# Kernel optimization log

Hardware: AMD Instinct MI355X
Metric: run time of the kernel (lower is better)

## Reference

```python
import jax, jax.numpy as jnp
import numpy as np

B, S, H = 2, 4096, 1024
NH, BS, NR = 16, 64, 3
HD = H // NH
NB = S // BS
PEN = -10000.0


def setup_inputs():
    key = jax.random.key(0)
    k0, k1, k2, k3 = jax.random.split(key, 4)
    s = 0.02
    inp = {
        'hidden_states': jax.random.normal(k0, (B, S, H), jnp.float32),
        'attention_mask': jnp.ones((B, S), jnp.float32),
        'Wq': jax.random.normal(k1, (H, H), jnp.float32) * s,
        'Wk': jax.random.normal(k2, (H, H), jnp.float32) * s,
        'Wv': jax.random.normal(k3, (H, H), jnp.float32) * s,
        'bq': jnp.zeros((H,), jnp.float32),
        'bk': jnp.zeros((H,), jnp.float32),
        'bv': jnp.zeros((H,), jnp.float32),
    }
    rng = np.random.default_rng(0)
    inp['rand_attn'] = jnp.asarray(rng.integers(1, NB - 1, size=(B, NH, NB - 2, NR)), jnp.int32)
    return inp


def _attend(q_blk, kmat, vmat, mask, rsd):
    # q_blk:[b,h,q,d]  kmat/vmat:[b,h,k,d]  mask: multiplicative {0,1} broadcastable to [b,h,q,k]
    p = jnp.einsum('bhqd,bhkd->bhqk', q_blk, kmat) * rsd + (1.0 - mask) * PEN
    return jnp.einsum('bhqk,bhkd->bhqd', jax.nn.softmax(p, axis=-1), vmat)


def reference(hidden_states, attention_mask, Wq, bq, Wk, bk, Wv, bv, rand_attn):
    b, s, _ = hidden_states.shape
    h, d, bs = NH, HD, BS
    nb = s // bs
    rsd = 1.0 / jnp.sqrt(jnp.asarray(d, hidden_states.dtype))

    def proj(W, bias):
        return (hidden_states @ W + bias).reshape(b, s, h, d).transpose(0, 2, 1, 3)

    q, k, v = proj(Wq, bq), proj(Wk, bk), proj(Wv, bv)  # [b,h,s,d]

    # --- masks (create_masks_for_block_sparse_attn)
    bm = attention_mask.reshape(b, nb, bs)
    band_mask = jnp.einsum('blq,blk->blqk', bm[:, 2:-2],
                           jnp.concatenate([bm[:, 1:-3], bm[:, 2:-2], bm[:, 3:-1]], axis=2))[:, None]
    from_mask = attention_mask.reshape(b, 1, s, 1)
    to_mask = attention_mask.reshape(b, 1, 1, s)

    qb = q.reshape(b, h, nb, bs, d)
    kb = k.reshape(b, h, nb, bs, d)
    vb = v.reshape(b, h, nb, bs, d)

    # --- gather random blocks (jax_gather with batch_dims=2)
    gather2 = jax.vmap(jax.vmap(lambda m, i: m[i]))
    gk = gather2(kb, rand_attn).reshape(b, h, nb - 2, NR * bs, d)
    gv = gather2(vb, rand_attn).reshape(b, h, nb - 2, NR * bs, d)
    rm = jax.vmap(lambda m, i: m[i])(bm, rand_attn).reshape(b, h, nb - 2, NR * bs)
    rand_mask = jnp.einsum('blq,bhlk->bhlqk', bm[:, 1:-1], rm)  # [b,h,nb-2,bs,NR*bs]

    # --- block 0: attends to everything
    first_ctx = _attend(qb[:, :, 0], k, v, to_mask, rsd)[:, :, None]

    # --- block 1: first 3 blocks + last block + its random blocks
    ones_r = jnp.ones((b, 1, 1, NR * bs), q.dtype)
    sk = jnp.concatenate([kb[:, :, 0], kb[:, :, 1], kb[:, :, 2], kb[:, :, -1], gk[:, :, 0]], axis=2)
    sv = jnp.concatenate([vb[:, :, 0], vb[:, :, 1], vb[:, :, 2], vb[:, :, -1], gv[:, :, 0]], axis=2)
    seq_pad = jnp.concatenate([to_mask[:, :, :, :3 * bs], to_mask[:, :, :, -bs:], ones_r], axis=3)
    rand_pad = jnp.concatenate([jnp.ones((b, h, bs, 4 * bs), q.dtype), rand_mask[:, :, 0]], axis=3)
    second_ctx = _attend(qb[:, :, 1], sk, sv, jnp.minimum(seq_pad, rand_pad), rsd)[:, :, None]

    # --- middle blocks 2..nb-3: sliding band + random + first-global + last-global
    mq = qb[:, :, 2:-2]  # [b,h,L,bs,d], L = nb-4
    ek = jnp.concatenate([kb[:, :, 1:-3], kb[:, :, 2:-2], kb[:, :, 3:-1]], axis=3)  # [b,h,L,3bs,d]
    ev = jnp.concatenate([vb[:, :, 1:-3], vb[:, :, 2:-2], vb[:, :, 3:-1]], axis=3)
    band_p = jnp.einsum('bhlqd,bhlkd->bhlqk', mq, ek) * rsd + (1.0 - band_mask) * PEN
    rand_p = jnp.einsum('bhlqd,bhlkd->bhlqk', mq, gk[:, :, 1:-1]) * rsd + (1.0 - rand_mask[:, :, 1:-1]) * PEN
    first_p = jnp.einsum('bhlqd,bhkd->bhlqk', mq, kb[:, :, 0]) * rsd \
        + (1.0 - to_mask[:, :, :, :bs][:, :, :, None]) * PEN
    last_p = jnp.einsum('bhlqd,bhkd->bhlqk', mq, kb[:, :, -1]) * rsd \
        + (1.0 - to_mask[:, :, :, -bs:][:, :, :, None]) * PEN
    # scores layout: [first(bs) | band(3bs) | rand(NR*bs) | last(bs)]
    w = jax.nn.softmax(jnp.concatenate([first_p, band_p, rand_p, last_p], axis=-1), axis=-1)
    mid_ctx = jnp.einsum('bhlqk,bhlkd->bhlqd', w[..., bs:4 * bs], ev)
    mid_ctx += jnp.einsum('bhlqk,bhlkd->bhlqd', w[..., 4 * bs:-bs], gv[:, :, 1:-1])
    mid_ctx += jnp.einsum('bhlqk,bhkd->bhlqd', w[..., :bs], vb[:, :, 0])
    mid_ctx += jnp.einsum('bhlqk,bhkd->bhlqd', w[..., -bs:], vb[:, :, -1])

    # --- block nb-2: first block + last 3 blocks + its random blocks
    slk = jnp.concatenate([kb[:, :, 0], kb[:, :, -3], kb[:, :, -2], kb[:, :, -1], gk[:, :, -1]], axis=2)
    slv = jnp.concatenate([vb[:, :, 0], vb[:, :, -3], vb[:, :, -2], vb[:, :, -1], gv[:, :, -1]], axis=2)
    seq_pad = jnp.concatenate([to_mask[:, :, :, :bs], to_mask[:, :, :, -3 * bs:], ones_r], axis=3)
    rand_pad = jnp.concatenate([jnp.ones((b, h, bs, 4 * bs), q.dtype), rand_mask[:, :, -1]], axis=3)
    seclast_ctx = _attend(qb[:, :, -2], slk, slv, jnp.minimum(seq_pad, rand_pad), rsd)[:, :, None]

    # --- last block: attends to everything
    last_ctx = _attend(qb[:, :, -1], k, v, to_mask, rsd)[:, :, None]

    ctx = jnp.concatenate([first_ctx, second_ctx, mid_ctx, seclast_ctx, last_ctx], axis=2)
    ctx = ctx.reshape(b, h, s, d) * from_mask
    return ctx.transpose(0, 2, 1, 3).reshape(b, s, h * d)
```

## Files before the change

kernel.cpp:

```cpp
#include <hip/hip_runtime.h>

typedef unsigned short u16;
typedef short short8 __attribute__((ext_vector_type(8)));
typedef float f32x4 __attribute__((ext_vector_type(4)));

#define S_TOT 4096
#define NHEAD 16
#define HD 64
#define NB 64
#define BS 64
#define M0 16.0f

__device__ __forceinline__ u16 f2bf(float f) {
    unsigned int u = __builtin_bit_cast(unsigned int, f);
    unsigned int r = (u + 0x7fffu + ((u >> 16) & 1u)) >> 16;
    return (u16)r;
}

__device__ __forceinline__ void gload_lds16(const void* g, void* l) {
    __builtin_amdgcn_global_load_lds(
        (const __attribute__((address_space(1))) unsigned int*)g,
        (__attribute__((address_space(3))) unsigned int*)l, 16, 0, 0);
}

__device__ __forceinline__ float rsum16(float v) {
    v += __shfl_xor(v, 1);
    v += __shfl_xor(v, 2);
    v += __shfl_xor(v, 4);
    v += __shfl_xor(v, 8);
    return v;
}

__global__ __launch_bounds__(256) void convH(const float* __restrict__ h, u16* __restrict__ A) {
    size_t i = (size_t)blockIdx.x * blockDim.x + threadIdx.x;
    float4 v = ((const float4*)h)[i];
    ushort4 o;
    o.x = f2bf(v.x); o.y = f2bf(v.y); o.z = f2bf(v.z); o.w = f2bf(v.w);
    ((ushort4*)A)[i] = o;
}

__global__ __launch_bounds__(256) void transW(const float* __restrict__ Wq,
                                              const float* __restrict__ Wk,
                                              const float* __restrict__ Wv,
                                              u16* __restrict__ Wt) {
    const float* W = blockIdx.z == 0 ? Wq : (blockIdx.z == 1 ? Wk : Wv);
    u16* T = Wt + (size_t)blockIdx.z * 1024 * 1024;
    __shared__ float tile[64][65];
    int n0 = blockIdx.x * 64, k0 = blockIdx.y * 64;
    int tx = threadIdx.x, ty = threadIdx.y;
    for (int r = ty; r < 64; r += 4) tile[r][tx] = W[(size_t)(k0 + r) * 1024 + n0 + tx];
    __syncthreads();
    for (int r = ty; r < 64; r += 4) T[(size_t)(n0 + r) * 1024 + k0 + tx] = f2bf(tile[tx][r]);
}

__global__ __launch_bounds__(256, 2) void gemm_fused(const u16* __restrict__ Ah, const u16* __restrict__ Wt,
                                                     const float* __restrict__ bq, const float* __restrict__ bk,
                                                     const float* __restrict__ bv,
                                                     u16* __restrict__ Qb, u16* __restrict__ Kb,
                                                     u16* __restrict__ Vtb) {
    __shared__ alignas(16) char lds[2][32768];

    int bid = blockIdx.x;
    int xcd = bid & 7, idx = bid >> 3;
    int bm = xcd * 8 + (idx & 7);
    int bn = idx >> 3;
    int m0 = bm * 128, n0 = bn * 128;
    int mode = bn >> 3;
    const float* bias = mode == 0 ? bq : (mode == 1 ? bk : bv);
    int tid = threadIdx.x, wave = tid >> 6, lane = tid & 63;
    int lo = lane & 15, hi = lane >> 4;
    int wr = wave >> 1, wc = wave & 1;

    const char* Ac = (const char*)Ah;
    const char* Wc = (const char*)Wt;

    auto STAGE = [&](int buf, int t) {
#pragma unroll
        for (int i = 0; i < 4; i++) {
            int off = i * 4096 + tid * 16;
            int row = off >> 7, cb = off & 127;
            int cs = cb ^ ((row & 7) << 4);
            char* d = lds[buf] + i * 4096 + wave * 1024;
            gload_lds16(Ac + (size_t)(m0 + row) * 2048 + t * 128 + cs, d);
            gload_lds16(Wc + (size_t)(n0 + row) * 2048 + t * 128 + cs, d + 16384);
        }
    };

    f32x4 acc[4][4];
#pragma unroll
    for (int i = 0; i < 4; i++)
#pragma unroll
        for (int j = 0; j < 4; j++) acc[i][j] = f32x4{0.f, 0.f, 0.f, 0.f};

    STAGE(0, 0);
    asm volatile("s_waitcnt vmcnt(0)" ::: "memory");
    __builtin_amdgcn_s_barrier();
    __builtin_amdgcn_sched_barrier(0);

    for (int t = 0; t < 16; t++) {
        int buf = t & 1;
        if (t < 15) STAGE(buf ^ 1, t + 1);
        const char* As = lds[buf];
        const char* Bs = lds[buf] + 16384;
        short8 b[4][2];
#pragma unroll
        for (int ni = 0; ni < 4; ni++) {
            int row = wc * 64 + ni * 16 + lo;
            int sw = (row & 7) << 4;
#pragma unroll
            for (int kk = 0; kk < 2; kk++)
                b[ni][kk] = *(const short8*)(Bs + row * 128 + ((kk * 64 + hi * 16) ^ sw));
        }
        __builtin_amdgcn_s_setprio(1);
#pragma unroll
        for (int mi = 0; mi < 4; mi++) {
            int row = wr * 64 + mi * 16 + lo;
            int sw = (row & 7) << 4;
            short8 a0 = *(const short8*)(As + row * 128 + ((hi * 16) ^ sw));
            short8 a1 = *(const short8*)(As + row * 128 + ((64 + hi * 16) ^ sw));
#pragma unroll
            for (int ni = 0; ni < 4; ni++) {
                acc[mi][ni] = __builtin_amdgcn_mfma_f32_16x16x32_bf16(a0, b[ni][0], acc[mi][ni], 0, 0, 0);
                acc[mi][ni] = __builtin_amdgcn_mfma_f32_16x16x32_bf16(a1, b[ni][1], acc[mi][ni], 0, 0, 0);
            }
        }
        __builtin_amdgcn_s_setprio(0);
        asm volatile("s_waitcnt vmcnt(0)" ::: "memory");
        __builtin_amdgcn_s_barrier();
        __builtin_amdgcn_sched_barrier(0);
    }

    char* Cs = lds[0];
    int nb0 = n0 & 1023;
    float bv4[4];
#pragma unroll
    for (int ni = 0; ni < 4; ni++) bv4[ni] = bias[nb0 + wc * 64 + ni * 16 + lo];

    if (mode < 2) {
#pragma unroll
        for (int mi = 0; mi < 4; mi++)
#pragma unroll
            for (int ni = 0; ni < 4; ni++)
#pragma unroll
                for (int r = 0; r < 4; r++) {
                    int row = wr * 64 + mi * 16 + hi * 4 + r;
                    int nl = wc * 64 + ni * 16 + lo;
                    *(u16*)(Cs + ((row * 256 + nl * 2) ^ ((row & 7) << 4))) = f2bf(acc[mi][ni][r] + bv4[ni]);
                }
        __syncthreads();
        u16* T = (mode == 0) ? Qb : Kb;
#pragma unroll
        for (int it = 0; it < 8; it++) {
            int off = it * 4096 + tid * 16;
            int row = off >> 8, c = off & 255;
            short8 v = *(const short8*)(Cs + ((row * 256 + c) ^ ((row & 7) << 4)));
            int nm = nb0 + (c >> 1);
            int hh = nm >> 6, d = nm & 63;
            int s = m0 + row;
            int b_ = s >> 12, sr = s & 4095;
            *(short8*)&T[(((size_t)b_ * NHEAD + hh) * S_TOT + sr) * HD + d] = v;
        }
    } else {
#pragma unroll
        for (int mi = 0; mi < 4; mi++)
#pragma unroll
            for (int ni = 0; ni < 4; ni++)
#pragma unroll
                for (int r = 0; r < 4; r++) {
                    int row = wc * 64 + ni * 16 + lo;
                    int ml = wr * 64 + mi * 16 + hi * 4 + r;
                    *(u16*)(Cs + ((row * 256 + ml * 2) ^ ((row & 7) << 4))) = f2bf(acc[mi][ni][r] + bv4[ni]);
                }
        __syncthreads();
#pragma unroll
        for (int it = 0; it < 8; it++) {
            int off = it * 4096 + tid * 16;
            int row = off >> 8, c = off & 255;
            short8 v = *(const short8*)(Cs + ((row * 256 + c) ^ ((row & 7) << 4)));
            int dr = nb0 + row;
            int hh = dr >> 6, d = dr & 63;
            int s = m0 + (c >> 1);
            int b_ = s >> 12, sr = s & 4095;
            *(short8*)&Vtb[(((size_t)b_ * NHEAD + hh) * HD + d) * S_TOT + sr] = v;
        }
    }
}

__global__ __launch_bounds__(256) void bigbird_attn(const u16* __restrict__ Qb, const u16* __restrict__ Kb,
                                                    const u16* __restrict__ Vtb, const float* __restrict__ am,
                                                    const int* __restrict__ rand_attn, float* __restrict__ out,
                                                    float* __restrict__ po, float* __restrict__ pl) {
    int pid = blockIdx.x;
    int xcd = pid & 7, slot = pid >> 3;
    int bh = xcd * 4 + slot / 78;
    int lx = slot % 78;
    int b = bh >> 4, h = bh & 15;
    bool heavy = lx < 16;
    int p = lx & 7;
    int l = heavy ? ((lx >> 3) ? 63 : 0) : (lx - 15);
    const u16* Qh = Qb + (size_t)bh * S_TOT * HD;
    const u16* Kh = Kb + (size_t)bh * S_TOT * HD;
    const u16* Vh = Vtb + (size_t)bh * HD * S_TOT;
    int tid = threadIdx.x, wave = tid >> 6, lane = tid & 63;
    int lo = lane & 15, hi = lane >> 4;

    __shared__ int klist[64];
    __shared__ int knum_s;
    __shared__ alignas(16) u16 Kls[3][64 * 64];
    __shared__ alignas(16) u16 Vls[2][64 * 64];
    __shared__ alignas(16) u16 Plds[4][16 * 64];

    auto SK = [&](int s_, int kblk) {
        const char* Kc = (const char*)(Kh + (size_t)kblk * BS * HD);
#pragma unroll
        for (int i = 0; i < 2; i++) {
            int off = i * 4096 + wave * 1024 + lane * 16;
            int row = off >> 7, c = off & 127;
            gload_lds16(Kc + row * 128 + (c ^ ((row & 7) << 4)), (char*)Kls[s_] + i * 4096 + wave * 1024);
        }
    };
    auto SV = [&](int s_, int kblk) {
        const char* Vc = (const char*)(Vh + kblk * BS);
#pragma unroll
        for (int i = 0; i < 2; i++) {
            int off = i * 4096 + wave * 1024 + lane * 16;
            int row = off >> 7, c = off & 127;
            gload_lds16(Vc + (size_t)row * 8192 + (c ^ ((row & 7) << 4)), (char*)Vls[s_] + i * 4096 + wave * 1024);
        }
    };

    if (tid == 0) {
        if (heavy) {
            for (int i = 0; i < 8; i++) klist[i] = p * 8 + i;
            knum_s = 8;
        } else {
            int q = 0;
            klist[q++] = 0;
            if (l == 1) { klist[q++] = 1; klist[q++] = 2; }
            else if (l == 62) { klist[q++] = 61; klist[q++] = 62; }
            else { klist[q++] = l - 1; klist[q++] = l; klist[q++] = l + 1; }
            klist[q++] = 63;
            const int* ra = rand_attn + (((size_t)b * NHEAD + h) * 62 + (l - 1)) * 3;
            klist[q++] = ra[0]; klist[q++] = ra[1]; klist[q++] = ra[2];
            knum_s = q;
        }
    }
    int c0 = heavy ? p * 8 : 0;
    SK(0, c0);
    SV(0, c0);
    __syncthreads();
    int kn = knum_s;
    int qrow = l * BS + wave * 16;
    if (1 < kn) SK(1, klist[1]);

    short8 qf[2];
#pragma unroll
    for (int kk = 0; kk < 2; kk++)
        qf[kk] = *(const short8*)&Qh[(size_t)(qrow + lo) * HD + kk * 32 + hi * 8];

    float ls[4];
    f32x4 oacc[4];
#pragma unroll
    for (int r = 0; r < 4; r++) ls[r] = 0.f;
#pragma unroll
    for (int n = 0; n < 4; n++) oacc[n] = f32x4{0.f, 0.f, 0.f, 0.f};
    char* pbase = (char*)&Plds[wave][0];

    for (int ci = 0; ci < kn; ci++) {
        int kbase = klist[ci] * BS;
        if (ci + 1 < kn) SV((ci + 1) & 1, klist[ci + 1]);
        if (ci + 2 < kn) SK((ci + 2) % 3, klist[ci + 2]);
        const char* Kc = (const char*)Kls[ci % 3];
        const char* Vc = (const char*)Vls[ci & 1];
        float pen[4];
#pragma unroll
        for (int t = 0; t < 4; t++) pen[t] = (1.0f - am[b * S_TOT + kbase + t * 16 + lo]) * (-10000.0f) - M0;
        f32x4 sc[4];
#pragma unroll
        for (int t = 0; t < 4; t++) {
            f32x4 c = f32x4{0.f, 0.f, 0.f, 0.f};
#pragma unroll
            for (int kk = 0; kk < 2; kk++) {
                int kr = t * 16 + lo;
                int a = (kr * 128 + kk * 64 + hi * 16) ^ ((kr & 7) << 4);
                short8 kf = *(const short8*)(Kc + a);
                c = __builtin_amdgcn_mfma_f32_16x16x32_bf16(qf[kk], kf, c, 0, 0, 0);
            }
            sc[t] = c;
        }
#pragma unroll
        for (int t = 0; t < 4; t++)
#pragma unroll
            for (int r = 0; r < 4; r++) {
                float pr = __expf(sc[t][r] * 0.125f + pen[t]);
                ls[r] += pr;
                int row = hi * 4 + r, col = t * 16 + lo;
                int off = (row * 128 + col * 2) ^ ((row & 7) << 4);
                *(u16*)(pbase + off) = f2bf(pr);
            }
#pragma unroll
        for (int kk = 0; kk < 2; kk++) {
            int off = (lo * 128 + kk * 64 + hi * 16) ^ ((lo & 7) << 4);
            short8 pf = *(const short8*)(pbase + off);
#pragma unroll
            for (int n = 0; n < 4; n++) {
                int vr = n * 16 + lo;
                int a = (vr * 128 + kk * 64 + hi * 16) ^ ((vr & 7) << 4);
                short8 vf = *(const short8*)(Vc + a);
                oacc[n] = __builtin_amdgcn_mfma_f32_16x16x32_bf16(pf, vf, oacc[n], 0, 0, 0);
            }
        }
        if (ci + 1 < kn) {
            if (ci + 2 < kn) {
                asm volatile("s_waitcnt vmcnt(2)" ::: "memory");
            } else {
                asm volatile("s_waitcnt vmcnt(0)" ::: "memory");
            }
            __builtin_amdgcn_s_barrier();
            __builtin_amdgcn_sched_barrier(0);
        }
    }

    if (heavy) {
        int combo = (bh << 1) | (l ? 1 : 0);
        int base = (combo * 8 + p) * 64;
#pragma unroll
        for (int r = 0; r < 4; r++) {
            int qr = wave * 16 + hi * 4 + r;
            float lsum = rsum16(ls[r]);
            if (lo == 0) pl[base + qr] = lsum;
#pragma unroll
            for (int n = 0; n < 4; n++)
                po[(size_t)(base + qr) * 64 + n * 16 + lo] = oacc[n][r];
        }
    } else {
#pragma unroll
        for (int r = 0; r < 4; r++) {
            float lsum = rsum16(ls[r]);
            int q = qrow + hi * 4 + r;
            float qm = am[b * S_TOT + q];
            float iv = qm / lsum;
#pragma unroll
            for (int n = 0; n < 4; n++)
                out[((size_t)b * S_TOT + q) * 1024 + h * HD + n * 16 + lo] = oacc[n][r] * iv;
        }
    }
}

__global__ __launch_bounds__(256) void reduce_heavy(const float* __restrict__ po, const float* __restrict__ pl,
                                                    const float* __restrict__ am, float* __restrict__ out) {
    int combo = blockIdx.x;
    int b = combo >> 5, h = (combo >> 1) & 15, hv = combo & 1;
    int l = hv ? 63 : 0;
    for (int idx = threadIdx.x; idx < 4096; idx += 256) {
        int qr = idx >> 6, d = idx & 63;
        float s = 0.f, lsum = 0.f;
#pragma unroll
        for (int p = 0; p < 8; p++) {
            s += po[(size_t)((combo * 8 + p) * 64 + qr) * 64 + d];
            lsum += pl[(combo * 8 + p) * 64 + qr];
        }
        int q = l * BS + qr;
        float qm = am[b * S_TOT + q];
        out[((size_t)b * S_TOT + q) * 1024 + h * HD + d] = s / lsum * qm;
    }
}

extern "C" void kernel_launch(void* const* d_in, const int* in_sizes, int n_in,
                              void* d_out, int out_size, void* d_ws, size_t ws_size,
                              hipStream_t stream) {
    const float* hidden = (const float*)d_in[0];
    const float* am = (const float*)d_in[1];
    const float* Wq = (const float*)d_in[2];
    const float* Wk = (const float*)d_in[3];
    const float* Wv = (const float*)d_in[4];
    const float* bq = (const float*)d_in[5];
    const float* bk = (const float*)d_in[6];
    const float* bv = (const float*)d_in[7];
    const int* rand_attn = (const int*)d_in[8];
    float* out = (float*)d_out;

    char* w = (char*)d_ws;
    u16* Ah = (u16*)w;  w += (size_t)8192 * 1024 * 2;
    u16* Wt = (u16*)w;  w += (size_t)3 * 1024 * 1024 * 2;
    u16* Qb = (u16*)w;  w += (size_t)2 * 16 * 4096 * 64 * 2;
    u16* Kb = (u16*)w;  w += (size_t)2 * 16 * 4096 * 64 * 2;
    u16* Vtb = (u16*)w;
    float* po = (float*)Ah;
    float* pl = po + (size_t)64 * 8 * 64 * 64;

    convH<<<8192, 256, 0, stream>>>(hidden, Ah);
    transW<<<dim3(16, 16, 3), dim3(64, 4), 0, stream>>>(Wq, Wk, Wv, Wt);
    gemm_fused<<<1536, 256, 0, stream>>>(Ah, Wt, bq, bk, bv, Qb, Kb, Vtb);
    bigbird_attn<<<2496, 256, 0, stream>>>(Qb, Kb, Vtb, am, rand_attn, out, po, pl);
    reduce_heavy<<<64, 256, 0, stream>>>(po, pl, am, out);
}
```

Measured before the change: 140.1 us.

## Widen QKV GEMM tile to 128x256 with 8 waves and triple-buffered LDS

The fused QKV projection GEMM now uses 512-thread blocks with a 128x256 output tile, halving the grid to 768 blocks. This raises reuse of each A tile across more weight columns. The K loop moves from double to triple buffering, staging two tiles ahead and waiting with a partial vmcnt so global-to-LDS loads overlap more MFMA work. The cost is 144KB of LDS per block, which leaves room for only one block per CU and shrinks the number of resident waves available to hide latency.

```diff
diff --git a/kernel.cpp b/kernel.cpp
--- a/kernel.cpp
+++ b/kernel.cpp
@@ -53,36 +53,42 @@
     for (int r = ty; r < 64; r += 4) T[(size_t)(n0 + r) * 1024 + k0 + tx] = f2bf(tile[tx][r]);
 }
 
-__global__ __launch_bounds__(256, 2) void gemm_fused(const u16* __restrict__ Ah, const u16* __restrict__ Wt,
+__global__ __launch_bounds__(512, 2) void gemm_fused(const u16* __restrict__ Ah, const u16* __restrict__ Wt,
                                                      const float* __restrict__ bq, const float* __restrict__ bk,
                                                      const float* __restrict__ bv,
                                                      u16* __restrict__ Qb, u16* __restrict__ Kb,
                                                      u16* __restrict__ Vtb) {
-    __shared__ alignas(16) char lds[2][32768];
+    __shared__ alignas(16) char lds[3 * 49152];
 
     int bid = blockIdx.x;
     int xcd = bid & 7, idx = bid >> 3;
     int bm = xcd * 8 + (idx & 7);
     int bn = idx >> 3;
-    int m0 = bm * 128, n0 = bn * 128;
-    int mode = bn >> 3;
+    int m0 = bm * 128, n0 = bn * 256;
+    int mode = bn >> 2;
     const float* bias = mode == 0 ? bq : (mode == 1 ? bk : bv);
     int tid = threadIdx.x, wave = tid >> 6, lane = tid & 63;
     int lo = lane & 15, hi = lane >> 4;
-    int wr = wave >> 1, wc = wave & 1;
+    int wr = wave >> 2, wc = wave & 3;
 
     const char* Ac = (const char*)Ah;
     const char* Wc = (const char*)Wt;
 
-    auto STAGE = [&](int buf, int t) {
-#pragma unroll
-        for (int i = 0; i < 4; i++) {
-            int off = i * 4096 + tid * 16;
+    auto STAGE = [&](int slot, int t) {
+        char* sb = lds + slot * 49152;
+#pragma unroll
+        for (int i = 0; i < 2; i++) {
+            int off = i * 8192 + tid * 16;
             int row = off >> 7, cb = off & 127;
             int cs = cb ^ ((row & 7) << 4);
-            char* d = lds[buf] + i * 4096 + wave * 1024;
-            gload_lds16(Ac + (size_t)(m0 + row) * 2048 + t * 128 + cs, d);
-            gload_lds16(Wc + (size_t)(n0 + row) * 2048 + t * 128 + cs, d + 16384);
+            gload_lds16(Ac + (size_t)(m0 + row) * 2048 + t * 128 + cs, sb + i * 8192 + wave * 1024);
+        }
+#pragma unroll
+        for (int i = 0; i < 4; i++) {
+            int off = i * 8192 + tid * 16;
+            int row = off >> 7, cb = off & 127;
+            int cs = cb ^ ((row & 7) << 4);
+            gload_lds16(Wc + (size_t)(n0 + row) * 2048 + t * 128 + cs, sb + 16384 + i * 8192 + wave * 1024);
         }
     };
 
@@ -96,12 +102,13 @@
     asm volatile("s_waitcnt vmcnt(0)" ::: "memory");
     __builtin_amdgcn_s_barrier();
     __builtin_amdgcn_sched_barrier(0);
+    STAGE(1, 1);
 
     for (int t = 0; t < 16; t++) {
-        int buf = t & 1;
-        if (t < 15) STAGE(buf ^ 1, t + 1);
-        const char* As = lds[buf];
-        const char* Bs = lds[buf] + 16384;
+        int slot = t % 3;
+        if (t + 2 < 16) STAGE((t + 2) % 3, t + 2);
+        const char* As = lds + slot * 49152;
+        const char* Bs = As + 16384;
         short8 b[4][2];
 #pragma unroll
         for (int ni = 0; ni < 4; ni++) {
@@ -125,12 +132,19 @@
             }
         }
         __builtin_amdgcn_s_setprio(0);
-        asm volatile("s_waitcnt vmcnt(0)" ::: "memory");
-        __builtin_amdgcn_s_barrier();
-        __builtin_amdgcn_sched_barrier(0);
-    }
-
-    char* Cs = lds[0];
+        if (t + 1 < 16) {
+            if (t + 2 < 16) {
+                asm volatile("s_waitcnt vmcnt(6)" ::: "memory");
+            } else {
+                asm volatile("s_waitcnt vmcnt(0)" ::: "memory");
+            }
+            __builtin_amdgcn_s_barrier();
+            __builtin_amdgcn_sched_barrier(0);
+        }
+    }
+    __syncthreads();
+
+    char* Cs = lds;
     int nb0 = n0 & 1023;
     float bv4[4];
 #pragma unroll
@@ -145,15 +159,15 @@
                 for (int r = 0; r < 4; r++) {
                     int row = wr * 64 + mi * 16 + hi * 4 + r;
                     int nl = wc * 64 + ni * 16 + lo;
-                    *(u16*)(Cs + ((row * 256 + nl * 2) ^ ((row & 7) << 4))) = f2bf(acc[mi][ni][r] + bv4[ni]);
+                    *(u16*)(Cs + ((row * 512 + nl * 2) ^ ((row & 7) << 4))) = f2bf(acc[mi][ni][r] + bv4[ni]);
                 }
         __syncthreads();
         u16* T = (mode == 0) ? Qb : Kb;
 #pragma unroll
         for (int it = 0; it < 8; it++) {
-            int off = it * 4096 + tid * 16;
-            int row = off >> 8, c = off & 255;
-            short8 v = *(const short8*)(Cs + ((row * 256 + c) ^ ((row & 7) << 4)));
+            int off = it * 8192 + tid * 16;
+            int row = off >> 9, c = off & 511;
+            short8 v = *(const short8*)(Cs + ((row * 512 + c) ^ ((row & 7) << 4)));
             int nm = nb0 + (c >> 1);
             int hh = nm >> 6, d = nm & 63;
             int s = m0 + row;
@@ -174,7 +188,7 @@
         __syncthreads();
 #pragma unroll
         for (int it = 0; it < 8; it++) {
-            int off = it * 4096 + tid * 16;
+            int off = it * 8192 + tid * 16;
             int row = off >> 8, c = off & 255;
             short8 v = *(const short8*)(Cs + ((row * 256 + c) ^ ((row & 7) << 4)));
             int dr = nb0 + row;
@@ -391,7 +405,7 @@
 
     convH<<<8192, 256, 0, stream>>>(hidden, Ah);
     transW<<<dim3(16, 16, 3), dim3(64, 4), 0, stream>>>(Wq, Wk, Wv, Wt);
-    gemm_fused<<<1536, 256, 0, stream>>>(Ah, Wt, bq, bk, bv, Qb, Kb, Vtb);
+    gemm_fused<<<768, 512, 0, stream>>>(Ah, Wt, bq, bk, bv, Qb, Kb, Vtb);
     bigbird_attn<<<2496, 256, 0, stream>>>(Qb, Kb, Vtb, am, rand_attn, out, po, pl);
     reduce_heavy<<<64, 256, 0, stream>>>(po, pl, am, out);
 }
```

Result: no change. 142.1 us (+1.4%).

## Split attention into mid and heavy kernels, finer heavy split, precompute mask penalties

Applied to the files above, without the earlier changes.

Splits the single attention kernel into a specialized mid-block kernel and a heavy (global first/last block) kernel. The heavy query blocks are now split 16 ways with 4 key blocks each instead of 8 ways with 8, and the reduction is widened to match. Mask penalties are precomputed into LDS once per block instead of being loaded from global memory inside the loop. This removes branch divergence and uneven work per block, but adds an extra kernel launch and more partial-result traffic. The heavy partials now reuse the weight scratch buffer.

```diff
diff --git a/kernel.cpp b/kernel.cpp
--- a/kernel.cpp
+++ b/kernel.cpp
@@ -186,26 +186,23 @@
     }
 }
 
-__global__ __launch_bounds__(256) void bigbird_attn(const u16* __restrict__ Qb, const u16* __restrict__ Kb,
-                                                    const u16* __restrict__ Vtb, const float* __restrict__ am,
-                                                    const int* __restrict__ rand_attn, float* __restrict__ out,
-                                                    float* __restrict__ po, float* __restrict__ pl) {
+__global__ __launch_bounds__(256) void bigbird_mid(const u16* __restrict__ Qb, const u16* __restrict__ Kb,
+                                                   const u16* __restrict__ Vtb, const float* __restrict__ am,
+                                                   const int* __restrict__ rand_attn, float* __restrict__ out) {
     int pid = blockIdx.x;
     int xcd = pid & 7, slot = pid >> 3;
-    int bh = xcd * 4 + slot / 78;
-    int lx = slot % 78;
+    int bh = xcd * 4 + slot / 62;
+    int l = slot % 62 + 1;
     int b = bh >> 4, h = bh & 15;
-    bool heavy = lx < 16;
-    int p = lx & 7;
-    int l = heavy ? ((lx >> 3) ? 63 : 0) : (lx - 15);
     const u16* Qh = Qb + (size_t)bh * S_TOT * HD;
     const u16* Kh = Kb + (size_t)bh * S_TOT * HD;
     const u16* Vh = Vtb + (size_t)bh * HD * S_TOT;
     int tid = threadIdx.x, wave = tid >> 6, lane = tid & 63;
     int lo = lane & 15, hi = lane >> 4;
-
-    __shared__ int klist[64];
-    __shared__ int knum_s;
+    int kn = (l == 1 || l == 62) ? 7 : 8;
+
+    __shared__ int klist[8];
+    __shared__ float pen_lds[8][64];
     __shared__ alignas(16) u16 Kls[3][64 * 64];
     __shared__ alignas(16) u16 Vls[2][64 * 64];
     __shared__ alignas(16) u16 Plds[4][16 * 64];
@@ -229,30 +226,31 @@
         }
     };
 
+    SK(0, 0);
+    SV(0, 0);
     if (tid == 0) {
-        if (heavy) {
-            for (int i = 0; i < 8; i++) klist[i] = p * 8 + i;
-            knum_s = 8;
-        } else {
-            int q = 0;
-            klist[q++] = 0;
-            if (l == 1) { klist[q++] = 1; klist[q++] = 2; }
-            else if (l == 62) { klist[q++] = 61; klist[q++] = 62; }
-            else { klist[q++] = l - 1; klist[q++] = l; klist[q++] = l + 1; }
-            klist[q++] = 63;
-            const int* ra = rand_attn + (((size_t)b * NHEAD + h) * 62 + (l - 1)) * 3;
-            klist[q++] = ra[0]; klist[q++] = ra[1]; klist[q++] = ra[2];
-            knum_s = q;
-        }
-    }
-    int c0 = heavy ? p * 8 : 0;
-    SK(0, c0);
-    SV(0, c0);
+        int q = 0;
+        klist[q++] = 0;
+        if (l == 1) { klist[q++] = 1; klist[q++] = 2; }
+        else if (l == 62) { klist[q++] = 61; klist[q++] = 62; }
+        else { klist[q++] = l - 1; klist[q++] = l; klist[q++] = l + 1; }
+        klist[q++] = 63;
+        const int* ra = rand_attn + (((size_t)b * NHEAD + h) * 62 + (l - 1)) * 3;
+        klist[q++] = ra[0]; klist[q++] = ra[1]; klist[q++] = ra[2];
+    }
     __syncthreads();
-    int kn = knum_s;
+
+#pragma unroll
+    for (int it = 0; it < 2; it++) {
+        int idx = it * 256 + tid;
+        int ci = idx >> 6, col = idx & 63;
+        if (ci < kn)
+            pen_lds[ci][col] = (1.0f - am[b * S_TOT + klist[ci] * BS + col]) * (-10000.0f) - M0;
+    }
+    SK(1, klist[1]);
+    __syncthreads();
+
     int qrow = l * BS + wave * 16;
-    if (1 < kn) SK(1, klist[1]);
-
     short8 qf[2];
 #pragma unroll
     for (int kk = 0; kk < 2; kk++)
@@ -267,14 +265,13 @@
     char* pbase = (char*)&Plds[wave][0];
 
     for (int ci = 0; ci < kn; ci++) {
-        int kbase = klist[ci] * BS;
         if (ci + 1 < kn) SV((ci + 1) & 1, klist[ci + 1]);
         if (ci + 2 < kn) SK((ci + 2) % 3, klist[ci + 2]);
         const char* Kc = (const char*)Kls[ci % 3];
         const char* Vc = (const char*)Vls[ci & 1];
         float pen[4];
 #pragma unroll
-        for (int t = 0; t < 4; t++) pen[t] = (1.0f - am[b * S_TOT + kbase + t * 16 + lo]) * (-10000.0f) - M0;
+        for (int t = 0; t < 4; t++) pen[t] = pen_lds[ci][t * 16 + lo];
         f32x4 sc[4];
 #pragma unroll
         for (int t = 0; t < 4; t++) {
@@ -321,29 +318,147 @@
         }
     }
 
-    if (heavy) {
-        int combo = (bh << 1) | (l ? 1 : 0);
-        int base = (combo * 8 + p) * 64;
-#pragma unroll
-        for (int r = 0; r < 4; r++) {
-            int qr = wave * 16 + hi * 4 + r;
-            float lsum = rsum16(ls[r]);
-            if (lo == 0) pl[base + qr] = lsum;
-#pragma unroll
-            for (int n = 0; n < 4; n++)
-                po[(size_t)(base + qr) * 64 + n * 16 + lo] = oacc[n][r];
-        }
-    } else {
-#pragma unroll
-        for (int r = 0; r < 4; r++) {
-            float lsum = rsum16(ls[r]);
-            int q = qrow + hi * 4 + r;
-            float qm = am[b * S_TOT + q];
-            float iv = qm / lsum;
-#pragma unroll
-            for (int n = 0; n < 4; n++)
-                out[((size_t)b * S_TOT + q) * 1024 + h * HD + n * 16 + lo] = oacc[n][r] * iv;
-        }
+#pragma unroll
+    for (int r = 0; r < 4; r++) {
+        float lsum = rsum16(ls[r]);
+        int q = qrow + hi * 4 + r;
+        float qm = am[b * S_TOT + q];
+        float iv = qm / lsum;
+#pragma unroll
+        for (int n = 0; n < 4; n++)
+            out[((size_t)b * S_TOT + q) * 1024 + h * HD + n * 16 + lo] = oacc[n][r] * iv;
+    }
+}
+
+__global__ __launch_bounds__(256) void bigbird_heavy(const u16* __restrict__ Qb, const u16* __restrict__ Kb,
+                                                     const u16* __restrict__ Vtb, const float* __restrict__ am,
+                                                     float* __restrict__ po, float* __restrict__ pl) {
+    int pid = blockIdx.x;
+    int xcd = pid & 7, slot = pid >> 3;
+    int bh = xcd * 4 + (slot >> 5);
+    int rem = slot & 31;
+    int hv = rem >> 4, p = rem & 15;
+    int l = hv ? 63 : 0;
+    int b = bh >> 4;
+    const u16* Qh = Qb + (size_t)bh * S_TOT * HD;
+    const u16* Kh = Kb + (size_t)bh * S_TOT * HD;
+    const u16* Vh = Vtb + (size_t)bh * HD * S_TOT;
+    int tid = threadIdx.x, wave = tid >> 6, lane = tid & 63;
+    int lo = lane & 15, hi = lane >> 4;
+
+    __shared__ float pen_lds[4][64];
+    __shared__ alignas(16) u16 Kls[3][64 * 64];
+    __shared__ alignas(16) u16 Vls[2][64 * 64];
+    __shared__ alignas(16) u16 Plds[4][16 * 64];
+
+    auto SK = [&](int s_, int kblk) {
+        const char* Kc = (const char*)(Kh + (size_t)kblk * BS * HD);
+#pragma unroll
+        for (int i = 0; i < 2; i++) {
+            int off = i * 4096 + wave * 1024 + lane * 16;
+            int row = off >> 7, c = off & 127;
+            gload_lds16(Kc + row * 128 + (c ^ ((row & 7) << 4)), (char*)Kls[s_] + i * 4096 + wave * 1024);
+        }
+    };
+    auto SV = [&](int s_, int kblk) {
+        const char* Vc = (const char*)(Vh + kblk * BS);
+#pragma unroll
+        for (int i = 0; i < 2; i++) {
+            int off = i * 4096 + wave * 1024 + lane * 16;
+            int row = off >> 7, c = off & 127;
+            gload_lds16(Vc + (size_t)row * 8192 + (c ^ ((row & 7) << 4)), (char*)Vls[s_] + i * 4096 + wave * 1024);
+        }
+    };
+
+    int c0 = p * 4;
+    SK(0, c0);
+    SV(0, c0);
+    {
+        int ci = tid >> 6, col = tid & 63;
+        pen_lds[ci][col] = (1.0f - am[b * S_TOT + (c0 + ci) * BS + col]) * (-10000.0f) - M0;
+    }
+    SK(1, c0 + 1);
+    __syncthreads();
+
+    int qrow = l * BS + wave * 16;
+    short8 qf[2];
+#pragma unroll
+    for (int kk = 0; kk < 2; kk++)
+        qf[kk] = *(const short8*)&Qh[(size_t)(qrow + lo) * HD + kk * 32 + hi * 8];
+
+    float ls[4];
+    f32x4 oacc[4];
+#pragma unroll
+    for (int r = 0; r < 4; r++) ls[r] = 0.f;
+#pragma unroll
+    for (int n = 0; n < 4; n++) oacc[n] = f32x4{0.f, 0.f, 0.f, 0.f};
+    char* pbase = (char*)&Plds[wave][0];
+
+#pragma unroll
+    for (int ci = 0; ci < 4; ci++) {
+        if (ci + 1 < 4) SV((ci + 1) & 1, c0 + ci + 1);
+        if (ci + 2 < 4) SK((ci + 2) % 3, c0 + ci + 2);
+        const char* Kc = (const char*)Kls[ci % 3];
+        const char* Vc = (const char*)Vls[ci & 1];
+        float pen[4];
+#pragma unroll
+        for (int t = 0; t < 4; t++) pen[t] = pen_lds[ci][t * 16 + lo];
+        f32x4 sc[4];
+#pragma unroll
+        for (int t = 0; t < 4; t++) {
+            f32x4 c = f32x4{0.f, 0.f, 0.f, 0.f};
+#pragma unroll
+            for (int kk = 0; kk < 2; kk++) {
+                int kr = t * 16 + lo;
+                int a = (kr * 128 + kk * 64 + hi * 16) ^ ((kr & 7) << 4);
+                short8 kf = *(const short8*)(Kc + a);
+                c = __builtin_amdgcn_mfma_f32_16x16x32_bf16(qf[kk], kf, c, 0, 0, 0);
+            }
+            sc[t] = c;
+        }
+#pragma unroll
+        for (int t = 0; t < 4; t++)
+#pragma unroll
+            for (int r = 0; r < 4; r++) {
+                float pr = __expf(sc[t][r] * 0.125f + pen[t]);
+                ls[r] += pr;
+                int row = hi * 4 + r, col = t * 16 + lo;
+                int off = (row * 128 + col * 2) ^ ((row & 7) << 4);
+                *(u16*)(pbase + off) = f2bf(pr);
+            }
+#pragma unroll
+        for (int kk = 0; kk < 2; kk++) {
+            int off = (lo * 128 + kk * 64 + hi * 16) ^ ((lo & 7) << 4);
+            short8 pf = *(const short8*)(pbase + off);
+#pragma unroll
+            for (int n = 0; n < 4; n++) {
+                int vr = n * 16 + lo;
+                int a = (vr * 128 + kk * 64 + hi * 16) ^ ((vr & 7) << 4);
+                short8 vf = *(const short8*)(Vc + a);
+                oacc[n] = __builtin_amdgcn_mfma_f32_16x16x32_bf16(pf, vf, oacc[n], 0, 0, 0);
+            }
+        }
+        if (ci + 1 < 4) {
+            if (ci + 2 < 4) {
+                asm volatile("s_waitcnt vmcnt(2)" ::: "memory");
+            } else {
+                asm volatile("s_waitcnt vmcnt(0)" ::: "memory");
+            }
+            __builtin_amdgcn_s_barrier();
+            __builtin_amdgcn_sched_barrier(0);
+        }
+    }
+
+    int combo = (bh << 1) | hv;
+    int base = (combo * 16 + p) * 64;
+#pragma unroll
+    for (int r = 0; r < 4; r++) {
+        int qr = wave * 16 + hi * 4 + r;
+        float lsum = rsum16(ls[r]);
+        if (lo == 0) pl[base + qr] = lsum;
+#pragma unroll
+        for (int n = 0; n < 4; n++)
+            po[(size_t)(base + qr) * 64 + n * 16 + lo] = oacc[n][r];
     }
 }
 
@@ -356,9 +471,9 @@
         int qr = idx >> 6, d = idx & 63;
         float s = 0.f, lsum = 0.f;
 #pragma unroll
-        for (int p = 0; p < 8; p++) {
-            s += po[(size_t)((combo * 8 + p) * 64 + qr) * 64 + d];
-            lsum += pl[(combo * 8 + p) * 64 + qr];
+        for (int p = 0; p < 16; p++) {
+            s += po[(size_t)((combo * 16 + p) * 64 + qr) * 64 + d];
+            lsum += pl[(combo * 16 + p) * 64 + qr];
         }
         int q = l * BS + qr;
         float qm = am[b * S_TOT + q];
@@ -387,11 +502,12 @@
     u16* Kb = (u16*)w;  w += (size_t)2 * 16 * 4096 * 64 * 2;
     u16* Vtb = (u16*)w;
     float* po = (float*)Ah;
-    float* pl = po + (size_t)64 * 8 * 64 * 64;
+    float* pl = (float*)Wt;
 
     convH<<<8192, 256, 0, stream>>>(hidden, Ah);
     transW<<<dim3(16, 16, 3), dim3(64, 4), 0, stream>>>(Wq, Wk, Wv, Wt);
     gemm_fused<<<1536, 256, 0, stream>>>(Ah, Wt, bq, bk, bv, Qb, Kb, Vtb);
-    bigbird_attn<<<2496, 256, 0, stream>>>(Qb, Kb, Vtb, am, rand_attn, out, po, pl);
+    bigbird_mid<<<1984, 256, 0, stream>>>(Qb, Kb, Vtb, am, rand_attn, out);
+    bigbird_heavy<<<1024, 256, 0, stream>>>(Qb, Kb, Vtb, am, po, pl);
     reduce_heavy<<<64, 256, 0, stream>>>(po, pl, am, out);
 }
```

Result: slower. 146.5 us (+4.6%).
